# Kernel optimization log

Measured on AMD Instinct MI355X. Metric: run time of the kernel, lower is better.

## Reference

```python
import jax, jax.numpy as jnp
import numpy as np

B, S, D, H = 4, 2048, 1024, 16
HD = D // H  # head_dim = 64


def setup_inputs() -> dict:
    key = jax.random.key(0)
    ks = jax.random.split(key, 5)
    scale = 0.02
    x = jax.random.normal(ks[0], (B, S, D), dtype=jnp.float32)
    Wq = jax.random.normal(ks[1], (D, D), dtype=jnp.float32) * scale
    Wk = jax.random.normal(ks[2], (D, D), dtype=jnp.float32) * scale
    Wv = jax.random.normal(ks[3], (D, D), dtype=jnp.float32) * scale
    Wo = jax.random.normal(ks[4], (D, D), dtype=jnp.float32) * scale
    # causal mask, broadcastable [1,1,S,S]; 0 entries get -10000 like masked_fill
    mask = jnp.tril(jnp.ones((S, S), dtype=jnp.int32))[None, None]
    return {"x": x, "Wq": Wq, "Wk": Wk, "Wv": Wv, "Wo": Wo, "mask": mask}


def reference(x, Wq, Wk, Wv, Wo, mask):
    b, s, _ = x.shape
    # nn.Linear: x @ W.T (no bias)
    q = (x @ Wq.T).reshape(b, s, H, HD).transpose(0, 2, 1, 3)  # [B,H,S,HD]
    k = (x @ Wk.T).reshape(b, s, H, HD).transpose(0, 2, 1, 3)
    v = (x @ Wv.T).reshape(b, s, H, HD).transpose(0, 2, 1, 3)
    attn = jnp.einsum('bhqd,bhkd->bhqk', q, k) / (HD ** 0.5)  # [B,H,S,S]
    attn = jnp.where(mask == 0, jnp.float32(-10000.0), attn)
    attn = jax.nn.softmax(attn, axis=-1)
    out = jnp.einsum('bhqk,bhkd->bhqd', attn, v)  # [B,H,S,HD]
    out = out.transpose(0, 2, 1, 3).reshape(b, s, H * HD)
    return out @ Wo.T
```

## Files before the change

### kernel.cpp

```cpp
#include <hip/hip_runtime.h>

typedef float    f4 __attribute__((ext_vector_type(4)));
typedef _Float16 h8 __attribute__((ext_vector_type(8)));
typedef _Float16 h4 __attribute__((ext_vector_type(4)));
typedef _Float16 h2 __attribute__((ext_vector_type(2)));

#define DEV static __device__ __forceinline__

DEV f4 mfma16(h8 a, h8 b, f4 c) {
  return __builtin_amdgcn_mfma_f32_16x16x32_f16(a, b, c, 0, 0, 0);
}

DEV void gload16(const void* g, void* lds) {
  __builtin_amdgcn_global_load_lds((__attribute__((address_space(1))) void*)g,
                                   (__attribute__((address_space(3))) void*)lds,
                                   16, 0, 0);
}

DEV h2 cvtpk(float a, float b) {
  return __builtin_bit_cast(h2, __builtin_amdgcn_cvt_pkrtz(a, b));
}

__global__ __launch_bounds__(256) void cvt_all(
    const float* __restrict__ x,  const float* __restrict__ wq,
    const float* __restrict__ wk, const float* __restrict__ wv,
    const float* __restrict__ wo,
    _Float16* __restrict__ xb, _Float16* __restrict__ wqkv, _Float16* __restrict__ wob)
{
  int b = blockIdx.x;
  const float* src; _Float16* dst; int i4;
  if      (b < 8192)  { src = x;  dst = xb;                 i4 = b * 256; }
  else if (b < 9216)  { src = wq; dst = wqkv;               i4 = (b - 8192)  * 256; }
  else if (b < 10240) { src = wk; dst = wqkv + (1u << 20);  i4 = (b - 9216)  * 256; }
  else if (b < 11264) { src = wv; dst = wqkv + (2u << 20);  i4 = (b - 10240) * 256; }
  else                { src = wo; dst = wob;                i4 = (b - 11264) * 256; }
  i4 += threadIdx.x;
  f4 v = ((const f4*)src)[i4];
  h4 o;
  o[0] = (_Float16)v[0]; o[1] = (_Float16)v[1];
  o[2] = (_Float16)v[2]; o[3] = (_Float16)v[3];
  ((h4*)dst)[i4] = o;
}

template<int MODE>
__global__ __launch_bounds__(256) void gemm_bt(
    const _Float16* __restrict__ A, const _Float16* __restrict__ Bt,
    float* __restrict__ C,
    _Float16* __restrict__ Qo, _Float16* __restrict__ Ko, _Float16* __restrict__ Vo,
    int N, int Ntiles)
{
  __shared__ _Float16 Al[128 * 32];
  __shared__ _Float16 Bl[128 * 32];
  const int K = 1024;
  int bid = blockIdx.x;
  int tm = bid / Ntiles, tn = bid - tm * Ntiles;
  int m0 = tm * 128, n0 = tn * 128;
  int t = threadIdx.x, w = t >> 6, l = t & 63, lo = l & 15, hi = l >> 4;
  int wr = w >> 1, wc = w & 1;

  const _Float16* Ag = A  + (size_t)(m0 + (t >> 2)) * K + (t & 3) * 8;
  const _Float16* Bg = Bt + (size_t)(n0 + (t >> 2)) * K + (t & 3) * 8;
  _Float16* Alw = Al + w * 512;
  _Float16* Blw = Bl + w * 512;

  f4 acc[4][4] = {};

  for (int k0 = 0; k0 < K; k0 += 32) {
    if (k0) __syncthreads();
    gload16(Ag + k0,          Alw);
    gload16(Ag + 64 * K + k0, Alw + 2048);
    gload16(Bg + k0,          Blw);
    gload16(Bg + 64 * K + k0, Blw + 2048);
    __syncthreads();
    h8 a[4], b[4];
    #pragma unroll
    for (int i = 0; i < 4; ++i)
      a[i] = *(const h8*)(Al + (wr * 64 + i * 16 + lo) * 32 + hi * 8);
    #pragma unroll
    for (int i = 0; i < 4; ++i)
      b[i] = *(const h8*)(Bl + (wc * 64 + i * 16 + lo) * 32 + hi * 8);
    #pragma unroll
    for (int mi = 0; mi < 4; ++mi)
      #pragma unroll
      for (int ni = 0; ni < 4; ++ni)
        acc[mi][ni] = mfma16(a[mi], b[ni], acc[mi][ni]);
  }

  #pragma unroll
  for (int mi = 0; mi < 4; ++mi) {
    #pragma unroll
    for (int ni = 0; ni < 4; ++ni) {
      #pragma unroll
      for (int j = 0; j < 4; ++j) {
        int row = m0 + wr * 64 + mi * 16 + hi * 4 + j;
        int col = n0 + wc * 64 + ni * 16 + lo;
        float v = acc[mi][ni][j];
        if (MODE == 0) {
          C[(size_t)row * N + col] = v;
        } else {
          int which = col >> 10;
          int cw = col & 1023;
          int hh = cw >> 6, hd = cw & 63;
          int bb = row >> 11, ss = row & 2047;
          if (which == 0) {
            Qo[(size_t)(bb * 16 + hh) * 131072 + (size_t)ss * 64 + hd] =
                (_Float16)(v * 0.1803368801111137f);
          } else if (which == 1) {
            Ko[(size_t)(bb * 16 + hh) * 131072 + (size_t)ss * 64 + hd] = (_Float16)v;
          } else {
            Vo[(size_t)(bb * 16 + hh) * 131072 + (size_t)hd * 2048 + ss] = (_Float16)v;
          }
        }
      }
    }
  }
}

__global__ __launch_bounds__(256, 3) void attn_kernel(
    const _Float16* __restrict__ Q, const _Float16* __restrict__ Kb,
    const _Float16* __restrict__ Vb, _Float16* __restrict__ O)
{
  __shared__ _Float16 Kl[2 * 4096];
  __shared__ _Float16 Vl[2 * 4096];
  __shared__ _Float16 Pl[4 * 2048];

  int bid = blockIdx.x;
  int bh = bid & 63, qi = 15 - (bid >> 6);
  int t = threadIdx.x, w = t >> 6, l = t & 63, lo = l & 15, hi = l >> 4;
  const size_t hoff = (size_t)bh * 131072;
  const _Float16* Kg = Kb + hoff;
  const _Float16* Vg = Vb + hoff;
  _Float16* Pw = Pl + w * 2048;
  int bb = bh >> 4, hh = bh & 15;
  int swz = (lo & 7) << 1;

  int rs = t >> 3, cs = t & 7;
  int sw_ = (cs ^ (rs & 7)) * 8;
  int srcK0 = rs * 64 + sw_,   srcK1 = srcK0 + 2048;
  int srcV0 = rs * 2048 + sw_, srcV1 = srcV0 + 65536;
  _Float16* kd0 = Kl + w * 512;
  _Float16* vd0 = Vl + w * 512;

  int koff[4][2], voff[2][4], pwoff[2][4], proff[2][2];
  #pragma unroll
  for (int kf = 0; kf < 4; ++kf) {
    int row = kf * 16 + lo;
    koff[kf][0] = row * 64 + ((hi       ^ (row & 7)) * 8);
    koff[kf][1] = row * 64 + (((4 + hi) ^ (row & 7)) * 8);
  }
  #pragma unroll
  for (int ks = 0; ks < 2; ++ks)
    #pragma unroll
    for (int df = 0; df < 4; ++df) {
      int row = df * 16 + lo;
      voff[ks][df] = row * 64 + ((((ks << 2) | hi) ^ (row & 7)) * 8);
    }
  #pragma unroll
  for (int m = 0; m < 2; ++m) {
    #pragma unroll
    for (int kf = 0; kf < 4; ++kf)
      pwoff[m][kf] = m * 1024 + lo * 64 + ((((kf << 2) | hi) ^ swz) * 4);
    #pragma unroll
    for (int ks = 0; ks < 2; ++ks)
      proff[m][ks] = m * 1024 + lo * 64 + ((((ks << 3) | (hi << 1)) ^ swz) * 4);
  }

  h8 ones;
  #pragma unroll
  for (int e = 0; e < 8; ++e) ones[e] = (_Float16)1.0f;

  int qb = qi * 128 + w * 32;
  const _Float16* Qp = Q + hoff + (size_t)(qb + lo) * 64 + hi * 8;
  h8 qf[2][2];
  qf[0][0] = *(const h8*)(Qp);
  qf[0][1] = *(const h8*)(Qp + 32);
  qf[1][0] = *(const h8*)(Qp + 1024);
  qf[1][1] = *(const h8*)(Qp + 1056);

  f4 acc[2][4] = {};
  float m_run[2] = {-1e30f, -1e30f};
  float l_run[2] = {0.f, 0.f};
  int nkt = 2 * qi + 2;

#define STAGE(buf, kt) do {                                                   \
    const _Float16* Kt_ = Kg + (size_t)(kt) * 4096;                           \
    const _Float16* Vt_ = Vg + (size_t)(kt) * 64;                             \
    gload16(Kt_ + srcK0, kd0 + (buf) * 4096);                                 \
    gload16(Kt_ + srcK1, kd0 + (buf) * 4096 + 2048);                          \
    gload16(Vt_ + srcV0, vd0 + (buf) * 4096);                                 \
    gload16(Vt_ + srcV1, vd0 + (buf) * 4096 + 2048);                          \
  } while (0)

#define ITER(kt, buf) do {                                                    \
    if ((kt) + 1 < nkt) STAGE(buf ^ 1, (kt) + 1);                             \
    const _Float16* Kc = Kl + (buf) * 4096;                                   \
    const _Float16* Vc = Vl + (buf) * 4096;                                   \
    f4 sc[2][4] = {};                                                         \
    __builtin_amdgcn_s_setprio(1);                                            \
    _Pragma("unroll")                                                         \
    for (int kf = 0; kf < 4; ++kf) {                                          \
      h8 k0 = *(const h8*)(Kc + koff[kf][0]);                                 \
      h8 k1 = *(const h8*)(Kc + koff[kf][1]);                                 \
      _Pragma("unroll")                                                       \
      for (int m = 0; m < 2; ++m) {                                           \
        sc[m][kf] = mfma16(k0, qf[m][0], sc[m][kf]);                          \
        sc[m][kf] = mfma16(k1, qf[m][1], sc[m][kf]);                          \
      }                                                                       \
    }                                                                         \
    __builtin_amdgcn_s_setprio(0);                                            \
    if ((kt) >= 2 * qi) {                                                     \
      _Pragma("unroll")                                                       \
      for (int m = 0; m < 2; ++m) {                                           \
        int qg = qb + m * 16 + lo;                                            \
        _Pragma("unroll")                                                     \
        for (int kf = 0; kf < 4; ++kf) {                                      \
          int kgb = (kt) * 64 + kf * 16 + hi * 4;                             \
          _Pragma("unroll")                                                   \
          for (int j = 0; j < 4; ++j)                                         \
            if (kgb + j > qg) sc[m][kf][j] = -1e30f;                          \
        }                                                                     \
      }                                                                       \
    }                                                                         \
    _Pragma("unroll")                                                         \
    for (int m = 0; m < 2; ++m) {                                             \
      f4 m4 = sc[m][0];                                                       \
      _Pragma("unroll")                                                       \
      for (int kf = 1; kf < 4; ++kf) {                                        \
        m4[0] = fmaxf(m4[0], sc[m][kf][0]); m4[1] = fmaxf(m4[1], sc[m][kf][1]);\
        m4[2] = fmaxf(m4[2], sc[m][kf][2]); m4[3] = fmaxf(m4[3], sc[m][kf][3]);\
      }                                                                       \
      float mx = fmaxf(fmaxf(m4[0], m4[1]), fmaxf(m4[2], m4[3]));             \
      if (!__all(mx <= m_run[m] + 8.f)) {           \
        mx = fmaxf(mx, __shfl_xor(mx, 16));                                   \
        mx = fmaxf(mx, __shfl_xor(mx, 32));                                   \
        float mn = fmaxf(m_run[m], mx);                                       \
        float cr = exp2f(m_run[m] - mn);                                      \
        m_run[m] = mn;                                                        \
        l_run[m] *= cr;                                                       \
        _Pragma("unroll")                                                     \
        for (int df = 0; df < 4; ++df) {                                      \
          acc[m][df][0] *= cr; acc[m][df][1] *= cr;                           \
          acc[m][df][2] *= cr; acc[m][df][3] *= cr;                           \
        }                                                                     \
      }                                                                       \
      float mn = m_run[m];                                                    \
      _Pragma("unroll")                                                       \
      for (int kf = 0; kf < 4; ++kf) {                                        \
        h4 pk;                                                                \
        pk.xy = cvtpk(exp2f(sc[m][kf][0] - mn), exp2f(sc[m][kf][1] - mn));    \
        pk.zw = cvtpk(exp2f(sc[m][kf][2] - mn), exp2f(sc[m][kf][3] - mn));    \
        *(h4*)(Pw + pwoff[m][kf]) = pk;                                       \
      }                                                                       \
    }                                                                         \
    __builtin_amdgcn_sched_barrier(0);                                        \
    asm volatile("s_waitcnt lgkmcnt(0)" ::: "memory");                        \
    __builtin_amdgcn_sched_barrier(0);                                        \
    f4 ls[2] = {};                                                            \
    __builtin_amdgcn_s_setprio(1);                                            \
    _Pragma("unroll")                                                         \
    for (int ks = 0; ks < 2; ++ks) {                                          \
      h8 pf[2];                                                               \
      _Pragma("unroll")                                                       \
      for (int m = 0; m < 2; ++m) {                                           \
        pf[m] = *(const h8*)(Pw + proff[m][ks]);                              \
        ls[m] = mfma16(ones, pf[m], ls[m]);                                   \
      }                                                                       \
      _Pragma("unroll")                                                       \
      for (int df = 0; df < 4; ++df) {                                        \
        h8 vf = *(const h8*)(Vc + voff[ks][df]);                              \
        _Pragma("unroll")                                                     \
        for (int m = 0; m < 2; ++m)                                           \
          acc[m][df] = mfma16(vf, pf[m], acc[m][df]);                         \
      }                                                                       \
    }                                                                         \
    __builtin_amdgcn_s_setprio(0);                                            \
    l_run[0] += ls[0][0];                                                     \
    l_run[1] += ls[1][0];                                                     \
    asm volatile("s_waitcnt vmcnt(0)" ::: "memory");                          \
    __syncthreads();                                                          \
  } while (0)

  STAGE(0, 0);
  asm volatile("s_waitcnt vmcnt(0)" ::: "memory");
  __syncthreads();

  for (int kt = 0; kt < nkt; kt += 2) {
    ITER(kt, 0);
    ITER(kt + 1, 1);
  }

  #pragma unroll
  for (int m = 0; m < 2; ++m) {
    float inv = 1.0f / l_run[m];
    int q = qb + m * 16 + lo;
    _Float16* Op = O + ((size_t)(bb * 2048 + q)) * 1024 + hh * 64 + (hi << 2);
    #pragma unroll
    for (int df = 0; df < 4; ++df) {
      h4 o4;
      o4[0] = (_Float16)(acc[m][df][0] * inv);
      o4[1] = (_Float16)(acc[m][df][1] * inv);
      o4[2] = (_Float16)(acc[m][df][2] * inv);
      o4[3] = (_Float16)(acc[m][df][3] * inv);
      *(h4*)(Op + df * 16) = o4;
    }
  }
#undef ITER
#undef STAGE
}

extern "C" void kernel_launch(void* const* d_in, const int* in_sizes, int n_in,
                              void* d_out, int out_size, void* d_ws, size_t ws_size,
                              hipStream_t stream)
{
  const float* x  = (const float*)d_in[0];
  const float* wq = (const float*)d_in[1];
  const float* wk = (const float*)d_in[2];
  const float* wv = (const float*)d_in[3];
  const float* wo = (const float*)d_in[4];

  char* ws = (char*)d_ws;
  _Float16* xb   = (_Float16*)(ws);
  _Float16* wqkv = (_Float16*)(ws + (16u << 20));
  _Float16* wob  = (_Float16*)(ws + (22u << 20));
  _Float16* Qb   = (_Float16*)(ws + (24u << 20));
  _Float16* Kb   = (_Float16*)(ws + (40u << 20));
  _Float16* Vb   = (_Float16*)(ws + (56u << 20));
  _Float16* Ob   = xb;

  cvt_all<<<12288, 256, 0, stream>>>(x, wq, wk, wv, wo, xb, wqkv, wob);
  gemm_bt<1><<<64 * 24, 256, 0, stream>>>(xb, wqkv, nullptr, Qb, Kb, Vb, 3072, 24);
  attn_kernel<<<1024, 256, 0, stream>>>(Qb, Kb, Vb, Ob);
  gemm_bt<0><<<64 * 8, 256, 0, stream>>>(Ob, wob, (float*)d_out,
                                         nullptr, nullptr, nullptr, 1024, 8);
}
```

Before: 200.0 us.

## Rewrite projection GEMMs with 256x128 tiles, triple-buffered LDS pipeline and swizzle

Both projection GEMMs are replaced by a 512-thread kernel with 256x128 tiles and a three-stage global-to-LDS ring buffer. Loads are issued two k-steps ahead and waited on with explicit vmcnt counts, so only one barrier is needed per step. The LDS layout is XOR-swizzled to avoid bank conflicts, blocks are remapped across the 8 XCDs, MFMA bursts run at raised wave priority, and V is stored as vectorized h4 writes. The aim is to hide global-load latency and improve MFMA utilization, at the cost of more LDS use and hand-tuned wait counts that are fragile.

```diff
diff --git a/kernel.cpp b/kernel.cpp
--- a/kernel.cpp
+++ b/kernel.cpp
@@ -43,75 +43,148 @@
 }
 
 template<int MODE>
-__global__ __launch_bounds__(256) void gemm_bt(
+__global__ __launch_bounds__(512) void gemm8(
     const _Float16* __restrict__ A, const _Float16* __restrict__ Bt,
     float* __restrict__ C,
     _Float16* __restrict__ Qo, _Float16* __restrict__ Ko, _Float16* __restrict__ Vo,
-    int N, int Ntiles)
+    int N, int Nt)
 {
-  __shared__ _Float16 Al[128 * 32];
-  __shared__ _Float16 Bl[128 * 32];
-  const int K = 1024;
+  __shared__ _Float16 Al[3][8192];
+  __shared__ _Float16 Bl[3][4096];
+  const int K = 1024, NT = 32;
+
   int bid = blockIdx.x;
-  int tm = bid / Ntiles, tn = bid - tm * Ntiles;
-  int m0 = tm * 128, n0 = tn * 128;
+  int cpx = gridDim.x >> 3;
+  bid = (bid & 7) * cpx + (bid >> 3);
+  int tm = bid / Nt, tn = bid - tm * Nt;
+  int m0 = tm * 256, n0 = tn * 128;
+
   int t = threadIdx.x, w = t >> 6, l = t & 63, lo = l & 15, hi = l >> 4;
-  int wr = w >> 1, wc = w & 1;
-
-  const _Float16* Ag = A  + (size_t)(m0 + (t >> 2)) * K + (t & 3) * 8;
-  const _Float16* Bg = Bt + (size_t)(n0 + (t >> 2)) * K + (t & 3) * 8;
-  _Float16* Alw = Al + w * 512;
-  _Float16* Blw = Bl + w * 512;
-
-  f4 acc[4][4] = {};
-
-  for (int k0 = 0; k0 < K; k0 += 32) {
-    if (k0) __syncthreads();
-    gload16(Ag + k0,          Alw);
-    gload16(Ag + 64 * K + k0, Alw + 2048);
-    gload16(Bg + k0,          Blw);
-    gload16(Bg + 64 * K + k0, Blw + 2048);
-    __syncthreads();
-    h8 a[4], b[4];
+  int wm = w >> 2, wn = w & 3;
+
+  int rA = t >> 2, cA = t & 3;
+  int csw = (cA ^ ((rA >> 1) & 3)) * 8;
+  const _Float16* Ag0 = A + (size_t)(m0 + rA) * K + csw;
+  const _Float16* Ag1 = Ag0 + (size_t)128 * K;
+  const _Float16* Bg  = Bt + (size_t)(n0 + rA) * K + csw;
+  _Float16* Ad = &Al[0][0] + w * 512;
+  _Float16* Bd = &Bl[0][0] + w * 512;
+
+  int swz = (lo >> 1) & 3;
+  int aoff[8], boff[2];
+  #pragma unroll
+  for (int mi = 0; mi < 8; ++mi)
+    aoff[mi] = (wm * 128 + mi * 16 + lo) * 32 + ((hi ^ swz) * 8);
+  #pragma unroll
+  for (int nf = 0; nf < 2; ++nf)
+    boff[nf] = (wn * 32 + nf * 16 + lo) * 32 + ((hi ^ swz) * 8);
+
+  f4 acc[8][2] = {};
+
+#define STAGE_A(buf, kt) do {                                  \
+    gload16(Ag0 + (kt) * 32, Ad + (buf) * 8192);               \
+    gload16(Ag1 + (kt) * 32, Ad + (buf) * 8192 + 4096);        \
+  } while (0)
+#define STAGE_B(buf, kt) do {                                  \
+    gload16(Bg + (kt) * 32, Bd + (buf) * 4096);                \
+  } while (0)
+
+  STAGE_A(0, 0); STAGE_B(0, 0);
+  STAGE_A(1, 1); STAGE_B(1, 1);
+
+  int cb = 0;
+  for (int kt = 0; kt < NT; ++kt) {
+    if (kt + 1 < NT) {
+      asm volatile("s_waitcnt vmcnt(3)" ::: "memory");
+    } else {
+      asm volatile("s_waitcnt vmcnt(0)" ::: "memory");
+    }
+    __builtin_amdgcn_sched_barrier(0);
+    __builtin_amdgcn_s_barrier();
+    __builtin_amdgcn_sched_barrier(0);
+
+    const _Float16* Ac = &Al[0][0] + cb * 8192;
+    const _Float16* Bc = &Bl[0][0] + cb * 4096;
+    int nb = cb + 2; if (nb >= 3) nb -= 3;
+
+    if (kt + 2 < NT) STAGE_A(nb, kt + 2);
+    h8 b0 = *(const h8*)(Bc + boff[0]);
+    h8 b1 = *(const h8*)(Bc + boff[1]);
+    h8 a0 = *(const h8*)(Ac + aoff[0]);
+    h8 a1 = *(const h8*)(Ac + aoff[1]);
+    h8 a2 = *(const h8*)(Ac + aoff[2]);
+    h8 a3 = *(const h8*)(Ac + aoff[3]);
+    __builtin_amdgcn_s_setprio(1);
+    acc[0][0] = mfma16(a0, b0, acc[0][0]); acc[0][1] = mfma16(a0, b1, acc[0][1]);
+    acc[1][0] = mfma16(a1, b0, acc[1][0]); acc[1][1] = mfma16(a1, b1, acc[1][1]);
+    acc[2][0] = mfma16(a2, b0, acc[2][0]); acc[2][1] = mfma16(a2, b1, acc[2][1]);
+    acc[3][0] = mfma16(a3, b0, acc[3][0]); acc[3][1] = mfma16(a3, b1, acc[3][1]);
+    __builtin_amdgcn_s_setprio(0);
+    __builtin_amdgcn_sched_barrier(0);
+
+    if (kt + 2 < NT) STAGE_B(nb, kt + 2);
+    h8 a4 = *(const h8*)(Ac + aoff[4]);
+    h8 a5 = *(const h8*)(Ac + aoff[5]);
+    h8 a6 = *(const h8*)(Ac + aoff[6]);
+    h8 a7 = *(const h8*)(Ac + aoff[7]);
+    __builtin_amdgcn_s_setprio(1);
+    acc[4][0] = mfma16(a4, b0, acc[4][0]); acc[4][1] = mfma16(a4, b1, acc[4][1]);
+    acc[5][0] = mfma16(a5, b0, acc[5][0]); acc[5][1] = mfma16(a5, b1, acc[5][1]);
+    acc[6][0] = mfma16(a6, b0, acc[6][0]); acc[6][1] = mfma16(a6, b1, acc[6][1]);
+    acc[7][0] = mfma16(a7, b0, acc[7][0]); acc[7][1] = mfma16(a7, b1, acc[7][1]);
+    __builtin_amdgcn_s_setprio(0);
+    __builtin_amdgcn_sched_barrier(0);
+
+    cb = cb + 1; if (cb == 3) cb = 0;
+  }
+#undef STAGE_A
+#undef STAGE_B
+
+  if (MODE == 0) {
     #pragma unroll
-    for (int i = 0; i < 4; ++i)
-      a[i] = *(const h8*)(Al + (wr * 64 + i * 16 + lo) * 32 + hi * 8);
-    #pragma unroll
-    for (int i = 0; i < 4; ++i)
-      b[i] = *(const h8*)(Bl + (wc * 64 + i * 16 + lo) * 32 + hi * 8);
-    #pragma unroll
-    for (int mi = 0; mi < 4; ++mi)
+    for (int mi = 0; mi < 8; ++mi)
       #pragma unroll
-      for (int ni = 0; ni < 4; ++ni)
-        acc[mi][ni] = mfma16(a[mi], b[ni], acc[mi][ni]);
-  }
-
-  #pragma unroll
-  for (int mi = 0; mi < 4; ++mi) {
-    #pragma unroll
-    for (int ni = 0; ni < 4; ++ni) {
+      for (int nf = 0; nf < 2; ++nf)
+        #pragma unroll
+        for (int j = 0; j < 4; ++j) {
+          int row = m0 + wm * 128 + mi * 16 + hi * 4 + j;
+          int col = n0 + wn * 32 + nf * 16 + lo;
+          C[(size_t)row * N + col] = acc[mi][nf][j];
+        }
+  } else {
+    int which = n0 >> 10;
+    int cb0 = (n0 & 1023) + wn * 32;
+    if (which == 2) {
       #pragma unroll
-      for (int j = 0; j < 4; ++j) {
-        int row = m0 + wr * 64 + mi * 16 + hi * 4 + j;
-        int col = n0 + wc * 64 + ni * 16 + lo;
-        float v = acc[mi][ni][j];
-        if (MODE == 0) {
-          C[(size_t)row * N + col] = v;
-        } else {
-          int which = col >> 10;
-          int cw = col & 1023;
-          int hh = cw >> 6, hd = cw & 63;
-          int bb = row >> 11, ss = row & 2047;
-          if (which == 0) {
-            Qo[(size_t)(bb * 16 + hh) * 131072 + (size_t)ss * 64 + hd] =
-                (_Float16)(v * 0.1803368801111137f);
-          } else if (which == 1) {
-            Ko[(size_t)(bb * 16 + hh) * 131072 + (size_t)ss * 64 + hd] = (_Float16)v;
-          } else {
-            Vo[(size_t)(bb * 16 + hh) * 131072 + (size_t)hd * 2048 + ss] = (_Float16)v;
-          }
+      for (int mi = 0; mi < 8; ++mi) {
+        int row0 = m0 + wm * 128 + mi * 16 + hi * 4;
+        int bb = row0 >> 11, ss0 = row0 & 2047;
+        #pragma unroll
+        for (int nf = 0; nf < 2; ++nf) {
+          int col = cb0 + nf * 16 + lo;
+          int hh = col >> 6, hd = col & 63;
+          h4 o4;
+          o4[0] = (_Float16)acc[mi][nf][0]; o4[1] = (_Float16)acc[mi][nf][1];
+          o4[2] = (_Float16)acc[mi][nf][2]; o4[3] = (_Float16)acc[mi][nf][3];
+          *(h4*)(Vo + (size_t)(bb * 16 + hh) * 131072 + (size_t)hd * 2048 + ss0) = o4;
         }
       }
+    } else {
+      _Float16* Dst = (which == 0) ? Qo : Ko;
+      float qs = (which == 0) ? 0.1803368801111137f : 1.0f;
+      #pragma unroll
+      for (int mi = 0; mi < 8; ++mi)
+        #pragma unroll
+        for (int nf = 0; nf < 2; ++nf)
+          #pragma unroll
+          for (int j = 0; j < 4; ++j) {
+            int row = m0 + wm * 128 + mi * 16 + hi * 4 + j;
+            int col = cb0 + nf * 16 + lo;
+            int hh = col >> 6, hd = col & 63;
+            int bb = row >> 11, ss = row & 2047;
+            Dst[(size_t)(bb * 16 + hh) * 131072 + (size_t)ss * 64 + hd] =
+                (_Float16)(acc[mi][nf][j] * qs);
+          }
     }
   }
 }
@@ -328,8 +401,8 @@
   _Float16* Ob   = xb;
 
   cvt_all<<<12288, 256, 0, stream>>>(x, wq, wk, wv, wo, xb, wqkv, wob);
-  gemm_bt<1><<<64 * 24, 256, 0, stream>>>(xb, wqkv, nullptr, Qb, Kb, Vb, 3072, 24);
+  gemm8<1><<<32 * 24, 512, 0, stream>>>(xb, wqkv, nullptr, Qb, Kb, Vb, 3072, 24);
   attn_kernel<<<1024, 256, 0, stream>>>(Qb, Kb, Vb, Ob);
-  gemm_bt<0><<<64 * 8, 256, 0, stream>>>(Ob, wob, (float*)d_out,
-                                         nullptr, nullptr, nullptr, 1024, 8);
-}
+  gemm8<0><<<32 * 8, 512, 0, stream>>>(Ob, wob, (float*)d_out,
+                                       nullptr, nullptr, nullptr, 1024, 8);
+}
```

Result: faster. 192.4 us (-3.8%).

## Rewrite projection GEMMs with larger tiles, swizzled LDS and software pipelining

Applied to the files above, without the earlier changes.

Replaces the 128x128, single-buffered, fully synchronised GEMM with a 512-thread kernel using 256x256 or 128x256 tiles, BK=64 with XOR-swizzled LDS, and double buffering with fine-grained vmcnt waits. MFMA work is interleaved with async global-to-LDS loads, and priority is raised around MFMA blocks. Blocks are remapped across XCDs for L2 locality, and the V transpose store is vectorised. The aim is to hide memory latency and cut barrier stalls in the QKV and output projections, at the cost of tricky hand-tuned wait counts and possible register pressure.

```diff
diff --git a/kernel.cpp b/kernel.cpp
--- a/kernel.cpp
+++ b/kernel.cpp
@@ -42,76 +42,176 @@
   ((h4*)dst)[i4] = o;
 }
 
-template<int MODE>
-__global__ __launch_bounds__(256) void gemm_bt(
+template<int MODE, int MF>
+__global__ __launch_bounds__(512) void gemmT(
     const _Float16* __restrict__ A, const _Float16* __restrict__ Bt,
     float* __restrict__ C,
     _Float16* __restrict__ Qo, _Float16* __restrict__ Ko, _Float16* __restrict__ Vo,
-    int N, int Ntiles)
+    int N, int Nt)
 {
-  __shared__ _Float16 Al[128 * 32];
-  __shared__ _Float16 Bl[128 * 32];
-  const int K = 1024;
+  constexpr int ASZ = MF * 16 * 64;
+  constexpr int BSZ = 8192;
+  constexpr int V1  = (MF == 8) ? 12 : 9;
+  constexpr int V2  = (MF == 8) ? 10 : 7;
+  constexpr int VL3 = (MF == 8) ? 8 : 6;
+  constexpr int VL5 = (MF == 8) ? 4 : 3;
+  constexpr int VL6 = (MF == 8) ? 2 : 1;
+  __shared__ _Float16 Al[4 * ASZ];
+  __shared__ _Float16 Bl[4 * BSZ];
+
   int bid = blockIdx.x;
-  int tm = bid / Ntiles, tn = bid - tm * Ntiles;
-  int m0 = tm * 128, n0 = tn * 128;
+  int cpx = gridDim.x >> 3;
+  bid = (bid & 7) * cpx + (bid >> 3);
+  int tm = bid / Nt, tn = bid - tm * Nt;
+  int m0 = tm * (MF * 32), n0 = tn * 256;
+
   int t = threadIdx.x, w = t >> 6, l = t & 63, lo = l & 15, hi = l >> 4;
-  int wr = w >> 1, wc = w & 1;
-
-  const _Float16* Ag = A  + (size_t)(m0 + (t >> 2)) * K + (t & 3) * 8;
-  const _Float16* Bg = Bt + (size_t)(n0 + (t >> 2)) * K + (t & 3) * 8;
-  _Float16* Alw = Al + w * 512;
-  _Float16* Blw = Bl + w * 512;
-
-  f4 acc[4][4] = {};
-
-  for (int k0 = 0; k0 < K; k0 += 32) {
-    if (k0) __syncthreads();
-    gload16(Ag + k0,          Alw);
-    gload16(Ag + 64 * K + k0, Alw + 2048);
-    gload16(Bg + k0,          Blw);
-    gload16(Bg + 64 * K + k0, Blw + 2048);
-    __syncthreads();
-    h8 a[4], b[4];
-    #pragma unroll
-    for (int i = 0; i < 4; ++i)
-      a[i] = *(const h8*)(Al + (wr * 64 + i * 16 + lo) * 32 + hi * 8);
-    #pragma unroll
-    for (int i = 0; i < 4; ++i)
-      b[i] = *(const h8*)(Bl + (wc * 64 + i * 16 + lo) * 32 + hi * 8);
-    #pragma unroll
-    for (int mi = 0; mi < 4; ++mi)
+  int wm = w >> 2, wn = w & 3;
+
+  int rsc = t >> 3;
+  int csrc = ((t & 7) ^ (rsc & 7)) * 8;
+  const _Float16 *As[2][2], *Bs[2][2];
+  #pragma unroll
+  for (int q = 0; q < 2; ++q) {
+    if (MF == 8) {
+      As[q][0] = A + (size_t)(m0 + q * 64 + rsc) * 1024 + csrc;
+      As[q][1] = A + (size_t)(m0 + 128 + q * 64 + rsc) * 1024 + csrc;
+    } else {
+      As[q][0] = A + (size_t)(m0 + (t >> 8) * 64 + q * 32 + (rsc & 31)) * 1024 + csrc;
+      As[q][1] = As[q][0];
+    }
+    #pragma unroll
+    for (int h = 0; h < 2; ++h)
+      Bs[q][h] = Bt + (size_t)(n0 + (2 * h + (t >> 8)) * 64 + q * 32 + (rsc & 31)) * 1024 + csrc;
+  }
+  _Float16* Adst = Al + w * 512;
+  _Float16* Bdst = Bl + w * 512;
+
+  int awoff = wm * (MF * 8 * 64) + lo * 64;
+  int bwoff = wn * 2048 + lo * 64;
+  int s0 = (hi ^ (lo & 7)) * 8;
+  int s1 = ((4 + hi) ^ (lo & 7)) * 8;
+
+  f4 acc[MF][4] = {};
+  h8 ar[MF / 2][2], br[2][2][2];
+
+#define VMW(n)  asm volatile("s_waitcnt vmcnt(%0)" :: "n"(n) : "memory")
+#define BARR    __builtin_amdgcn_s_barrier()
+#define LGKM0   do { asm volatile("s_waitcnt lgkmcnt(0)" ::: "memory"); \
+                     __builtin_amdgcn_sched_barrier(0); } while (0)
+#define STA(BUF, Q, KO) do { \
+    gload16(As[Q][0] + (KO), Adst + ((BUF) * 2 + (Q)) * ASZ); \
+    if (MF == 8) gload16(As[Q][1] + (KO), Adst + ((BUF) * 2 + (Q)) * ASZ + 4096); \
+  } while (0)
+#define STB(BUF, QN, KO) do { \
+    gload16(Bs[QN][0] + (KO), Bdst + ((BUF) * 2 + (QN)) * BSZ); \
+    gload16(Bs[QN][1] + (KO), Bdst + ((BUF) * 2 + (QN)) * BSZ + 4096); \
+  } while (0)
+#define RDA(BUF, Q) do { \
+    const _Float16* p_ = Al + ((BUF) * 2 + (Q)) * ASZ + awoff; \
+    _Pragma("unroll") \
+    for (int f_ = 0; f_ < MF / 2; ++f_) { \
+      ar[f_][0] = *(const h8*)(p_ + f_ * 1024 + s0); \
+      ar[f_][1] = *(const h8*)(p_ + f_ * 1024 + s1); } \
+  } while (0)
+#define RDB(BUF, QN, D) do { \
+    const _Float16* p_ = Bl + ((BUF) * 2 + (QN)) * BSZ + bwoff; \
+    br[D][0][0] = *(const h8*)(p_ + s0);        br[D][0][1] = *(const h8*)(p_ + s1); \
+    br[D][1][0] = *(const h8*)(p_ + 1024 + s0); br[D][1][1] = *(const h8*)(p_ + 1024 + s1); \
+  } while (0)
+#define MM(MH, D) do { \
+    __builtin_amdgcn_s_setprio(1); \
+    _Pragma("unroll") \
+    for (int f_ = 0; f_ < MF / 2; ++f_) \
+      _Pragma("unroll") \
+      for (int g_ = 0; g_ < 2; ++g_) { \
+        acc[(MH) * (MF / 2) + f_][(D) * 2 + g_] = \
+            mfma16(ar[f_][0], br[D][g_][0], acc[(MH) * (MF / 2) + f_][(D) * 2 + g_]); \
+        acc[(MH) * (MF / 2) + f_][(D) * 2 + g_] = \
+            mfma16(ar[f_][1], br[D][g_][1], acc[(MH) * (MF / 2) + f_][(D) * 2 + g_]); } \
+    __builtin_amdgcn_s_setprio(0); \
+    __builtin_amdgcn_sched_barrier(0); \
+  } while (0)
+
+  STA(0, 0, 0);  STB(0, 0, 0);  STB(0, 1, 0);  STA(0, 1, 0);
+  STA(1, 0, 64); STB(1, 0, 64); STB(1, 1, 64); STA(1, 1, 64);
+
+  int kof = 128;
+  #pragma unroll 1
+  for (int it = 0; it < 7; ++it) {
+    VMW(V1); BARR; RDA(0, 0); RDB(0, 0, 0); LGKM0; MM(0, 0);
+    VMW(V2); BARR; RDB(0, 1, 1); STA(0, 0, kof); STB(0, 0, kof); LGKM0; MM(0, 1);
+    VMW(V1); BARR; RDA(0, 1); STB(0, 1, kof); LGKM0; MM(1, 1);
+    BARR; STA(0, 1, kof); MM(1, 0);
+    VMW(V1); BARR; RDA(1, 0); RDB(1, 0, 0); LGKM0; MM(0, 0);
+    VMW(V2); BARR; RDB(1, 1, 1); STA(1, 0, kof + 64); STB(1, 0, kof + 64); LGKM0; MM(0, 1);
+    VMW(V1); BARR; RDA(1, 1); STB(1, 1, kof + 64); LGKM0; MM(1, 1);
+    BARR; STA(1, 1, kof + 64); MM(1, 0);
+    kof += 128;
+  }
+  VMW(V1);  BARR; RDA(0, 0); RDB(0, 0, 0); LGKM0; MM(0, 0);
+  VMW(V2);  BARR; RDB(0, 1, 1); LGKM0; MM(0, 1);
+  VMW(VL3); BARR; RDA(0, 1); LGKM0; MM(1, 1);
+  BARR; MM(1, 0);
+  VMW(VL5); BARR; RDA(1, 0); RDB(1, 0, 0); LGKM0; MM(0, 0);
+  VMW(VL6); BARR; RDB(1, 1, 1); LGKM0; MM(0, 1);
+  VMW(0);   BARR; RDA(1, 1); LGKM0; MM(1, 1);
+  BARR; MM(1, 0);
+
+#undef VMW
+#undef BARR
+#undef LGKM0
+#undef STA
+#undef STB
+#undef RDA
+#undef RDB
+#undef MM
+
+  if (MODE == 0) {
+    #pragma unroll
+    for (int mi = 0; mi < MF; ++mi)
       #pragma unroll
-      for (int ni = 0; ni < 4; ++ni)
-        acc[mi][ni] = mfma16(a[mi], b[ni], acc[mi][ni]);
-  }
-
-  #pragma unroll
-  for (int mi = 0; mi < 4; ++mi) {
-    #pragma unroll
-    for (int ni = 0; ni < 4; ++ni) {
+      for (int nf = 0; nf < 4; ++nf)
+        #pragma unroll
+        for (int j = 0; j < 4; ++j) {
+          int row = m0 + wm * (MF * 16) + mi * 16 + hi * 4 + j;
+          int col = n0 + wn * 64 + nf * 16 + lo;
+          C[(size_t)row * N + col] = acc[mi][nf][j];
+        }
+  } else {
+    int which = n0 >> 10;
+    int cb0 = (n0 & 1023) + wn * 64;
+    if (which == 2) {
       #pragma unroll
-      for (int j = 0; j < 4; ++j) {
-        int row = m0 + wr * 64 + mi * 16 + hi * 4 + j;
-        int col = n0 + wc * 64 + ni * 16 + lo;
-        float v = acc[mi][ni][j];
-        if (MODE == 0) {
-          C[(size_t)row * N + col] = v;
-        } else {
-          int which = col >> 10;
-          int cw = col & 1023;
-          int hh = cw >> 6, hd = cw & 63;
-          int bb = row >> 11, ss = row & 2047;
-          if (which == 0) {
-            Qo[(size_t)(bb * 16 + hh) * 131072 + (size_t)ss * 64 + hd] =
-                (_Float16)(v * 0.1803368801111137f);
-          } else if (which == 1) {
-            Ko[(size_t)(bb * 16 + hh) * 131072 + (size_t)ss * 64 + hd] = (_Float16)v;
-          } else {
-            Vo[(size_t)(bb * 16 + hh) * 131072 + (size_t)hd * 2048 + ss] = (_Float16)v;
-          }
+      for (int mi = 0; mi < MF; ++mi) {
+        int row0 = m0 + wm * (MF * 16) + mi * 16 + hi * 4;
+        int bb = row0 >> 11, ss0 = row0 & 2047;
+        #pragma unroll
+        for (int nf = 0; nf < 4; ++nf) {
+          int col = cb0 + nf * 16 + lo;
+          int hh = col >> 6, hd = col & 63;
+          h4 o4;
+          o4[0] = (_Float16)acc[mi][nf][0]; o4[1] = (_Float16)acc[mi][nf][1];
+          o4[2] = (_Float16)acc[mi][nf][2]; o4[3] = (_Float16)acc[mi][nf][3];
+          *(h4*)(Vo + (size_t)(bb * 16 + hh) * 131072 + (size_t)hd * 2048 + ss0) = o4;
         }
       }
+    } else {
+      _Float16* Dst = (which == 0) ? Qo : Ko;
+      float qs = (which == 0) ? 0.1803368801111137f : 1.0f;
+      #pragma unroll
+      for (int mi = 0; mi < MF; ++mi)
+        #pragma unroll
+        for (int nf = 0; nf < 4; ++nf)
+          #pragma unroll
+          for (int j = 0; j < 4; ++j) {
+            int row = m0 + wm * (MF * 16) + mi * 16 + hi * 4 + j;
+            int col = cb0 + nf * 16 + lo;
+            int hh = col >> 6, hd = col & 63;
+            int bb = row >> 11, ss = row & 2047;
+            Dst[(size_t)(bb * 16 + hh) * 131072 + (size_t)ss * 64 + hd] =
+                (_Float16)(acc[mi][nf][j] * qs);
+          }
     }
   }
 }
@@ -328,8 +428,8 @@
   _Float16* Ob   = xb;
 
   cvt_all<<<12288, 256, 0, stream>>>(x, wq, wk, wv, wo, xb, wqkv, wob);
-  gemm_bt<1><<<64 * 24, 256, 0, stream>>>(xb, wqkv, nullptr, Qb, Kb, Vb, 3072, 24);
+  gemmT<1, 8><<<32 * 12, 512, 0, stream>>>(xb, wqkv, nullptr, Qb, Kb, Vb, 3072, 12);
   attn_kernel<<<1024, 256, 0, stream>>>(Qb, Kb, Vb, Ob);
-  gemm_bt<0><<<64 * 8, 256, 0, stream>>>(Ob, wob, (float*)d_out,
-                                         nullptr, nullptr, nullptr, 1024, 8);
-}
+  gemmT<0, 4><<<64 * 4, 512, 0, stream>>>(Ob, wob, (float*)d_out,
+                                          nullptr, nullptr, nullptr, 1024, 4);
+}
```

After: 166.2 us. -16.9%, faster.
